# Kernel optimization log

Hardware: AMD Instinct MI355X
Metric: run time of the kernel (lower is better)

Reference implementation:

```python
import jax, jax.numpy as jnp
import numpy as np

N = 100000      # points
M = 12500       # cluster centers
E0 = 1600000    # point-level edges
E1 = 400000     # cluster-level edges
F_IN = 4        # raw point feature dim (e.g. intensity + extras)
D = 64          # hidden feature width
N_CLASSES = 8


def setup_inputs() -> dict:
    key = jax.random.key(0)
    ks = jax.random.split(key, 20)
    s = 0.05
    d = {}
    d["features"] = jax.random.normal(ks[0], (N, F_IN), jnp.float32)
    d["points"] = jax.random.normal(ks[1], (N, 3), jnp.float32)
    d["cluster_centers"] = jax.random.normal(ks[2], (M, 3), jnp.float32)
    d["l0_edges"] = jax.random.randint(ks[3], (E0, 2), 0, N)
    d["l1_edges"] = jax.random.randint(ks[4], (E1, 2), 0, M)
    d["labels"] = jax.random.randint(ks[5], (N,), 0, M)
    # Feature_extract MLP
    d["W_fe"] = s * jax.random.normal(ks[6], (F_IN + 3, D), jnp.float32)
    d["b_fe"] = jnp.zeros((D,), jnp.float32)
    # 4 Mini_GNN layers (layer2, layer2_1, layer6, layer6_1), stacked
    d["mini_We"] = s * jax.random.normal(ks[7], (4, D + 3, D), jnp.float32)
    d["mini_be"] = jnp.zeros((4, D), jnp.float32)
    d["mini_Wu"] = s * jax.random.normal(ks[8], (4, D, D), jnp.float32)
    d["mini_bu"] = jnp.zeros((4, D), jnp.float32)
    # Mini_to_Large
    d["W_m1"] = s * jax.random.normal(ks[9], (D + 3, D), jnp.float32)
    d["b_m1"] = jnp.zeros((D,), jnp.float32)
    d["W_m2"] = s * jax.random.normal(ks[10], (D, D), jnp.float32)
    d["b_m2"] = jnp.zeros((D,), jnp.float32)
    # 2 GNN layers on cluster graph (layer4, layer4_1), stacked
    d["gnn_We"] = s * jax.random.normal(ks[11], (2, D + 3, D), jnp.float32)
    d["gnn_be"] = jnp.zeros((2, D), jnp.float32)
    d["gnn_Wu"] = s * jax.random.normal(ks[12], (2, D, D), jnp.float32)
    d["gnn_bu"] = jnp.zeros((2, D), jnp.float32)
    # Large_to_Mini
    d["W_l"] = s * jax.random.normal(ks[13], (D + 3, D), jnp.float32)
    d["b_l"] = jnp.zeros((D,), jnp.float32)
    # Classifier
    d["W_c"] = s * jax.random.normal(ks[14], (D, N_CLASSES), jnp.float32)
    d["b_c"] = jnp.zeros((N_CLASSES,), jnp.float32)
    return d


def _gnn_layer(feat, pos, edges, We, be, Wu, bu, n_nodes):
    """PointGNN-style layer: gather -> edge MLP -> scatter max -> update MLP -> residual."""
    src, dst = edges[:, 0], edges[:, 1]
    e_in = jnp.concatenate([pos[src] - pos[dst], feat[src]], axis=-1)  # [E, 3+D]
    h = jax.nn.relu(e_in @ We + be)                                     # [E, D]
    agg = jax.ops.segment_max(h, dst, num_segments=n_nodes)            # [n, D]
    agg = jnp.where(jnp.isneginf(agg), 0.0, agg)  # nodes with no in-edges -> 0
    return jax.nn.relu(agg @ Wu + bu) + feat


def reference(features, points, cluster_centers, l0_edges, l1_edges, labels,
              W_fe, b_fe, mini_We, mini_be, mini_Wu, mini_bu,
              W_m1, b_m1, W_m2, b_m2, gnn_We, gnn_be, gnn_Wu, gnn_bu,
              W_l, b_l, W_c, b_c):
    rel = points - cluster_centers[labels]  # [N, 3] point pos relative to its cluster
    # layer1: Feature_extract
    f1 = jax.nn.relu(jnp.concatenate([features, rel], -1) @ W_fe + b_fe)
    # layer2 / layer2_1: Mini_GNN (scatter max) on point graph
    f2 = _gnn_layer(f1, points, l0_edges, mini_We[0], mini_be[0], mini_Wu[0], mini_bu[0], N)
    f2_1 = _gnn_layer(f2, points, l0_edges, mini_We[1], mini_be[1], mini_Wu[1], mini_bu[1], N)
    # layer3: Mini_to_Large (scatter sum by labels)
    h = jax.nn.relu(jnp.concatenate([f2_1, rel], -1) @ W_m1 + b_m1)
    c = jax.ops.segment_sum(h, labels, num_segments=M)  # [M, D]
    f3 = jax.nn.relu(c @ W_m2 + b_m2)
    # layer4 / layer4_1: GNN (scatter max) on cluster graph
    f4 = _gnn_layer(f3, cluster_centers, l1_edges, gnn_We[0], gnn_be[0], gnn_Wu[0], gnn_bu[0], M)
    f4_1 = _gnn_layer(f4, cluster_centers, l1_edges, gnn_We[1], gnn_be[1], gnn_Wu[1], gnn_bu[1], M)
    # layer5: Large_to_Mini (gather by labels)
    f5 = jax.nn.relu(jnp.concatenate([f4_1[labels], rel], -1) @ W_l + b_l)
    # layer6 / layer6_1 with residual skips per call()
    f6 = _gnn_layer(f5, points, l0_edges, mini_We[2], mini_be[2], mini_Wu[2], mini_bu[2], N)
    f6 = f6 + f2_1
    f6_1 = _gnn_layer(f6, points, l0_edges, mini_We[3], mini_be[3], mini_Wu[3], mini_bu[3], N)
    final = f6_1 + f2
    return final @ W_c + b_c  # [N, N_CLASSES] per-point logits
```

## Files before the change

kernel.cpp:

```cpp
#include <hip/hip_runtime.h>

#define N_PTS   100000
#define M_CL    12500
#define E0_N    1600000
#define E1_N    400000

#define NB      256
#define BIN_CAP 32
#define RANGE0  391
#define RANGE1  49
#define BCAP0   8192
#define BCAP1   2048

#define LSTR    72

typedef unsigned short ushortT;
typedef short  short8 __attribute__((ext_vector_type(8)));
typedef float  v4f    __attribute__((ext_vector_type(4)));
typedef _Float16 h2   __attribute__((ext_vector_type(2)));
typedef unsigned u4v  __attribute__((ext_vector_type(4)));

__device__ inline ushortT f2bf(float x){
  union{float f; unsigned u;} v; v.f = x;
  unsigned r = v.u + 0x7fffu + ((v.u >> 16) & 1u);
  return (ushortT)(r >> 16);
}
__device__ inline float bf2f(ushortT h){
  union{unsigned u; float f;} v; v.u = ((unsigned)h) << 16;
  return v.f;
}
__device__ inline ushortT f2h(float x){
  union{_Float16 h; ushortT u;} v; v.h = (_Float16)x;
  return v.u;
}
__device__ inline float h2f(ushortT u){
  union{ushortT u; _Float16 h;} v; v.u = u;
  return (float)v.h;
}
__device__ inline h2 pkmax(h2 a, h2 b){ return __builtin_elementwise_max(a, b); }
__device__ inline h2 u2h(unsigned u){ union{unsigned u; h2 h;} v{u}; return v.h; }


__global__ void k_binit(int* c0, int* c1){
  int t = threadIdx.x;
  c0[t] = t*BCAP0;
  c1[t] = t*BCAP1;
}

template<int RANGE>
__global__ __launch_bounds__(256) void k_bin(const int* __restrict__ edges, int E,
                                             int* __restrict__ bcur, unsigned* __restrict__ tmp){
  __shared__ unsigned stage[NB*BIN_CAP];
  __shared__ int scnt[NB];
  __shared__ int sbase[NB];
  int tid = threadIdx.x;
  int nchunks = (E + 2047) / 2048;
  for (int c = blockIdx.x; c < nchunks; c += gridDim.x){
    int base = c*2048;
    scnt[tid] = 0;
    __syncthreads();
    #pragma unroll
    for (int r=0;r<8;++r){
      int e = base + r*256 + tid;
      if (e < E){
        int s = edges[2*e], d = edges[2*e+1];
        int bk = d / RANGE;
        unsigned packed = ((unsigned)s << 11) | (unsigned)(d - bk*RANGE);
        int pos = atomicAdd(&scnt[bk], 1);
        if (pos < BIN_CAP) stage[bk*BIN_CAP+pos] = packed;
        else tmp[atomicAdd(&bcur[bk],1)] = packed;
      }
    }
    __syncthreads();
    {
      int nfl = scnt[tid]; if (nfl > BIN_CAP) nfl = BIN_CAP;
      sbase[tid] = atomicAdd(&bcur[tid], nfl);
    }
    __syncthreads();
    int wv = tid >> 6, ln = tid & 63;
    for (int bb=0; bb<32; ++bb){
      int bk = wv*64 + bb*2 + (ln>>5);
      int ent = ln & 31;
      int nf = scnt[bk]; if (nf > BIN_CAP) nf = BIN_CAP;
      if (ent < nf) tmp[sbase[bk]+ent] = stage[bk*BIN_CAP+ent];
    }
    __syncthreads();
  }
}

__global__ void k_scan_bases(const int* c0, int* bb0, int* off0e,
                             const int* c1, int* bb1, int* off1e){
  const int* cur = blockIdx.x ? c1 : c0;
  int* bb = blockIdx.x ? bb1 : bb0;
  int* offe = blockIdx.x ? off1e : off0e;
  int BC = blockIdx.x ? BCAP1 : BCAP0;
  int lane = threadIdx.x & 63;
  int base = lane*4;
  int v0 = cur[base+0] - (base+0)*BC;
  int v1 = cur[base+1] - (base+1)*BC;
  int v2 = cur[base+2] - (base+2)*BC;
  int v3 = cur[base+3] - (base+3)*BC;
  int psum = v0+v1+v2+v3, sc = psum;
  #pragma unroll
  for (int st=1; st<64; st<<=1){
    int x = __shfl_up(sc, st, 64);
    if (lane >= st) sc += x;
  }
  int ex = sc - psum;
  bb[base+0] = ex;
  bb[base+1] = ex + v0;
  bb[base+2] = ex + v0 + v1;
  bb[base+3] = ex + v0 + v1 + v2;
  if (lane == 63) *offe = sc;
}

template<int RANGE, int BCAP>
__global__ __launch_bounds__(256) void k_csr_build(const unsigned* __restrict__ tmp, const int* __restrict__ bcur,
                                                   const int* __restrict__ bb, int n,
                                                   int* __restrict__ offs, int* __restrict__ csr){
  constexpr int K = (RANGE + 255) / 256;
  __shared__ int hist[RANGE];
  __shared__ int part[256];
  int b = blockIdx.x, tid = threadIdx.x;
  int dlo = b*RANGE;
  int range = n - dlo; if (range > RANGE) range = RANGE; if (range < 0) range = 0;
  int cnt = bcur[b] - b*BCAP;
  for (int t=tid; t<RANGE; t+=256) hist[t] = 0;
  __syncthreads();
  const unsigned* sl = tmp + (size_t)b*BCAP;
  for (int j=tid; j<cnt; j+=256) atomicAdd(&hist[sl[j] & 2047u], 1);
  __syncthreads();
  int s = 0; int loc[K];
  #pragma unroll
  for (int kk=0; kk<K; ++kk){
    int idx = tid*K + kk;
    int v = (idx < RANGE) ? hist[idx] : 0;
    loc[kk] = s; s += v;
  }
  part[tid] = s; __syncthreads();
  int own = s;
  for (int st=1; st<256; st<<=1){
    int x = (tid >= st) ? part[tid-st] : 0;
    __syncthreads();
    part[tid] += x;
    __syncthreads();
  }
  int ebase = part[tid] - own;
  int gb = bb[b];
  __syncthreads();
  #pragma unroll
  for (int kk=0; kk<K; ++kk){
    int idx = tid*K + kk;
    if (idx < RANGE){
      int ex = ebase + loc[kk];
      if (idx < range) offs[dlo+idx] = gb + ex;
      hist[idx] = ex;
    }
  }
  __syncthreads();
  for (int j=tid; j<cnt; j+=256){
    unsigned p = sl[j];
    int pos = atomicAdd(&hist[p & 2047u], 1);
    csr[gb + pos] = (int)(p >> 11);
  }
}


__global__ __launch_bounds__(256) void k_count_lab(const int* __restrict__ labels, int n, int* __restrict__ cnt){
  int i = blockIdx.x*256 + threadIdx.x;
  if (i < n) atomicAdd(&cnt[labels[i]], 1);
}

__global__ __launch_bounds__(256) void k_chunk_sum(const int* __restrict__ cnt, int n, int* __restrict__ part){
  __shared__ int sd[256];
  int t = threadIdx.x, base = blockIdx.x*2048;
  int s = 0;
  #pragma unroll
  for (int r=0;r<8;++r){ int i = base + t*8 + r; if (i<n) s += cnt[i]; }
  sd[t]=s; __syncthreads();
  for (int st=128; st>0; st>>=1){ if (t<st) sd[t]+=sd[t+st]; __syncthreads(); }
  if (t==0) part[blockIdx.x]=sd[0];
}

__global__ void k_scan_part(int* part, int B, int* offs, int n){
  int lane = threadIdx.x & 63;
  int v = (lane < B) ? part[lane] : 0;
  int orig = v;
  #pragma unroll
  for (int st=1; st<64; st<<=1){
    int x = __shfl_up(v, st, 64);
    if (lane >= st) v += x;
  }
  if (lane < B) part[lane] = v - orig;
  if (lane == 63) offs[n] = v;
}

__global__ __launch_bounds__(256) void k_chunk_scan(const int* __restrict__ cnt, int n,
                                                    const int* __restrict__ part, int* __restrict__ offs){
  __shared__ int sd[256];
  int t=threadIdx.x, base=blockIdx.x*2048;
  int v[8]; int s=0;
  #pragma unroll
  for (int r=0;r<8;++r){ int i=base+t*8+r; v[r] = (i<n)?cnt[i]:0; s+=v[r]; }
  sd[t]=s; __syncthreads();
  for (int st=1; st<256; st<<=1){
    int x = (t>=st)? sd[t-st] : 0;
    __syncthreads();
    sd[t]+=x;
    __syncthreads();
  }
  int acc = part[blockIdx.x] + sd[t] - s;
  #pragma unroll
  for (int r=0;r<8;++r){ int i=base+t*8+r; if (i<n) offs[i]=acc; acc+=v[r]; }
}

__global__ __launch_bounds__(256) void k_fill_lab(const int* __restrict__ labels, int n,
                                                  const int* __restrict__ offs, int* __restrict__ cur,
                                                  int* __restrict__ csr){
  int i = blockIdx.x*256 + threadIdx.x;
  if (i < n){
    int d = labels[i];
    int p = atomicAdd(&cur[d], 1);
    csr[offs[d]+p] = i;
  }
}


struct WSrc { const float* p[16]; };

__global__ __launch_bounds__(256) void k_wprep(WSrc s, ushortT* __restrict__ wt, ushortT* __restrict__ wtc){
  int slot = blockIdx.x;
  if (slot < 15){
    const float* src = s.p[slot];
    ushortT* dst = wt + slot*4096;
    for (int e=threadIdx.x; e<4096; e+=256){
      int nn = e>>6, kk = e&63;
      dst[e] = f2bf(src[kk*64+nn]);
    }
  } else {
    const float* src = s.p[15];
    for (int e=threadIdx.x; e<1024; e+=256){
      int nn = e>>6, kk = e&63;
      wtc[e] = (nn<8) ? f2bf(src[kk*8+nn]) : (ushortT)0;
    }
  }
}


__global__ __launch_bounds__(256) void k_f1g(const float* __restrict__ features, const float* __restrict__ points,
                                             const float* __restrict__ centers, const int* __restrict__ labels,
                                             const float* __restrict__ W, const float* __restrict__ b,
                                             const ushortT* __restrict__ Wt2, const float* __restrict__ bias2,
                                             const float* __restrict__ Wr2,
                                             float* __restrict__ rel, ushortT* __restrict__ f1b,
                                             ushortT* __restrict__ gout, int n, int ntiles){
  __shared__ ushortT lds[4*16*LSTR];
  int tid = threadIdx.x;
  int lane = tid & 63, wslot = tid >> 6;
  int quad = lane >> 4, l15 = lane & 15;
  int gw = (blockIdx.x*256 + tid) >> 6;
  int nw = (gridDim.x*256) >> 6;
  float Wf0=W[0*64+lane], Wf1=W[1*64+lane], Wf2=W[2*64+lane], Wf3=W[3*64+lane];
  float wr0=W[4*64+lane], wr1=W[5*64+lane], wr2=W[6*64+lane];
  float bias=b[lane];
  short8 s0_0 = *(const short8*)(Wt2 + ( 0 + l15)*64 +  0 + quad*8);
  short8 s0_1 = *(const short8*)(Wt2 + ( 0 + l15)*64 + 32 + quad*8);
  short8 s1_0 = *(const short8*)(Wt2 + (16 + l15)*64 +  0 + quad*8);
  short8 s1_1 = *(const short8*)(Wt2 + (16 + l15)*64 + 32 + quad*8);
  short8 s2_0 = *(const short8*)(Wt2 + (32 + l15)*64 +  0 + quad*8);
  short8 s2_1 = *(const short8*)(Wt2 + (32 + l15)*64 + 32 + quad*8);
  short8 s3_0 = *(const short8*)(Wt2 + (48 + l15)*64 +  0 + quad*8);
  short8 s3_1 = *(const short8*)(Wt2 + (48 + l15)*64 + 32 + quad*8);
  float eb0 = bias2[l15], eb1 = bias2[16+l15], eb2 = bias2[32+l15], eb3 = bias2[48+l15];
  float e0c0=Wr2[0*64+l15], e0c1=Wr2[0*64+16+l15], e0c2=Wr2[0*64+32+l15], e0c3=Wr2[0*64+48+l15];
  float e1c0=Wr2[1*64+l15], e1c1=Wr2[1*64+16+l15], e1c2=Wr2[1*64+32+l15], e1c3=Wr2[1*64+48+l15];
  float e2c0=Wr2[2*64+l15], e2c1=Wr2[2*64+16+l15], e2c2=Wr2[2*64+32+l15], e2c3=Wr2[2*64+48+l15];

  for (int t=gw; t<ntiles; t+=nw){
    int i0 = t*16;
    for (int r=0;r<16;++r){
      int row = i0 + r;
      bool ok = row < n;
      int rr = ok ? row : n-1;
      int lb = labels[rr];
      float rx = points[rr*3+0]-centers[lb*3+0];
      float ry = points[rr*3+1]-centers[lb*3+1];
      float rz = points[rr*3+2]-centers[lb*3+2];
      float acc = bias + wr0*rx + wr1*ry + wr2*rz;
      acc += features[rr*4+0]*Wf0 + features[rr*4+1]*Wf1;
      acc += features[rr*4+2]*Wf2 + features[rr*4+3]*Wf3;
      acc = fmaxf(acc, 0.f);
      ushortT ab = f2bf(acc);
      if (ok){
        f1b[(size_t)row*64+lane] = ab;
        if (lane==0){ rel[row*3+0]=rx; rel[row*3+1]=ry; rel[row*3+2]=rz; }
      }
      lds[wslot*(16*LSTR) + r*LSTR + lane] = ab;
    }
    __builtin_amdgcn_wave_barrier();
    const ushortT* lp = lds + wslot*(16*LSTR) + l15*LSTR + quad*8;
    short8 sa0 = *(const short8*)(lp);
    short8 sa1 = *(const short8*)(lp + 32);
    __builtin_amdgcn_wave_barrier();
    v4f ec0 = {0.f,0.f,0.f,0.f}, ec1 = ec0, ec2 = ec0, ec3 = ec0;
    ec0 = __builtin_amdgcn_mfma_f32_16x16x32_bf16(sa0, s0_0, ec0, 0,0,0);
    ec1 = __builtin_amdgcn_mfma_f32_16x16x32_bf16(sa0, s1_0, ec1, 0,0,0);
    ec2 = __builtin_amdgcn_mfma_f32_16x16x32_bf16(sa0, s2_0, ec2, 0,0,0);
    ec3 = __builtin_amdgcn_mfma_f32_16x16x32_bf16(sa0, s3_0, ec3, 0,0,0);
    ec0 = __builtin_amdgcn_mfma_f32_16x16x32_bf16(sa1, s0_1, ec0, 0,0,0);
    ec1 = __builtin_amdgcn_mfma_f32_16x16x32_bf16(sa1, s1_1, ec1, 0,0,0);
    ec2 = __builtin_amdgcn_mfma_f32_16x16x32_bf16(sa1, s2_1, ec2, 0,0,0);
    ec3 = __builtin_amdgcn_mfma_f32_16x16x32_bf16(sa1, s3_1, ec3, 0,0,0);
    #pragma unroll
    for (int r=0;r<4;++r){
      int row = i0 + quad*4 + r;
      if (row < n){
        float vx=points[row*3+0], vy=points[row*3+1], vz=points[row*3+2];
        float g0 = ec0[r] + eb0 + vx*e0c0 + vy*e1c0 + vz*e2c0;
        float g1 = ec1[r] + eb1 + vx*e0c1 + vy*e1c1 + vz*e2c1;
        float g2 = ec2[r] + eb2 + vx*e0c2 + vy*e1c2 + vz*e2c2;
        float g3 = ec3[r] + eb3 + vx*e0c3 + vy*e1c3 + vz*e2c3;
        size_t base = (size_t)row*64 + l15;
        gout[base] = f2h(g0); gout[base+16] = f2h(g1); gout[base+32] = f2h(g2); gout[base+48] = f2h(g3);
      }
    }
  }
}


template<bool RELU, int NRES, bool USEREL, bool GATHER, bool OUT16, bool F16O, int EMODE, bool ERELU>
__global__ __launch_bounds__(256) void k_gemm(
    const ushortT* __restrict__ A, const ushortT* __restrict__ Wt,
    const float* __restrict__ bias, const float* __restrict__ Wr,
    const float* __restrict__ rel, const int* __restrict__ gidx,
    const ushortT* __restrict__ r1, const ushortT* __restrict__ r2,
    ushortT* __restrict__ out16,
    const ushortT* __restrict__ Wt2, const float* __restrict__ bias2,
    const float* __restrict__ Wr2, const float* __restrict__ vec2,
    void* __restrict__ eout,
    int n, int ntiles)
{
  constexpr int LDSZ = (EMODE>0) ? 4*16*LSTR : 4;
  __shared__ ushortT lds[LDSZ];
  int tid = threadIdx.x;
  int lane = tid & 63, wslot = tid >> 6;
  int quad = lane >> 4, l15 = lane & 15;
  int gw = (blockIdx.x*256 + tid) >> 6;
  int nw = (gridDim.x*256) >> 6;

  short8 bfr0_0 = *(const short8*)(Wt + ( 0 + l15)*64 +  0 + quad*8);
  short8 bfr0_1 = *(const short8*)(Wt + ( 0 + l15)*64 + 32 + quad*8);
  short8 bfr1_0 = *(const short8*)(Wt + (16 + l15)*64 +  0 + quad*8);
  short8 bfr1_1 = *(const short8*)(Wt + (16 + l15)*64 + 32 + quad*8);
  short8 bfr2_0 = *(const short8*)(Wt + (32 + l15)*64 +  0 + quad*8);
  short8 bfr2_1 = *(const short8*)(Wt + (32 + l15)*64 + 32 + quad*8);
  short8 bfr3_0 = *(const short8*)(Wt + (48 + l15)*64 +  0 + quad*8);
  short8 bfr3_1 = *(const short8*)(Wt + (48 + l15)*64 + 32 + quad*8);
  float bs0 = bias[ 0 + l15], bs1 = bias[16 + l15];
  float bs2 = bias[32 + l15], bs3 = bias[48 + l15];
  float w0c0=0,w0c1=0,w0c2=0,w0c3=0, w1c0=0,w1c1=0,w1c2=0,w1c3=0, w2c0=0,w2c1=0,w2c2=0,w2c3=0;
  if (USEREL){
    w0c0=Wr[0*64+l15]; w0c1=Wr[0*64+16+l15]; w0c2=Wr[0*64+32+l15]; w0c3=Wr[0*64+48+l15];
    w1c0=Wr[1*64+l15]; w1c1=Wr[1*64+16+l15]; w1c2=Wr[1*64+32+l15]; w1c3=Wr[1*64+48+l15];
    w2c0=Wr[2*64+l15]; w2c1=Wr[2*64+16+l15]; w2c2=Wr[2*64+32+l15]; w2c3=Wr[2*64+48+l15];
  }

  short8 s0_0{}, s0_1{}, s1_0{}, s1_1{}, s2_0{}, s2_1{}, s3_0{}, s3_1{};
  float eb0=0, eb1=0, eb2=0, eb3=0;
  float e0c0=0,e0c1=0,e0c2=0,e0c3=0, e1c0=0,e1c1=0,e1c2=0,e1c3=0, e2c0=0,e2c1=0,e2c2=0,e2c3=0;
  float ebias_c = 0.f;
  if (EMODE == 1){
    s0_0 = *(const short8*)(Wt2 + ( 0 + l15)*64 +  0 + quad*8);
    s0_1 = *(const short8*)(Wt2 + ( 0 + l15)*64 + 32 + quad*8);
    s1_0 = *(const short8*)(Wt2 + (16 + l15)*64 +  0 + quad*8);
    s1_1 = *(const short8*)(Wt2 + (16 + l15)*64 + 32 + quad*8);
    s2_0 = *(const short8*)(Wt2 + (32 + l15)*64 +  0 + quad*8);
    s2_1 = *(const short8*)(Wt2 + (32 + l15)*64 + 32 + quad*8);
    s3_0 = *(const short8*)(Wt2 + (48 + l15)*64 +  0 + quad*8);
    s3_1 = *(const short8*)(Wt2 + (48 + l15)*64 + 32 + quad*8);
    eb0 = bias2[l15]; eb1 = bias2[16+l15]; eb2 = bias2[32+l15]; eb3 = bias2[48+l15];
    e0c0=Wr2[0*64+l15]; e0c1=Wr2[0*64+16+l15]; e0c2=Wr2[0*64+32+l15]; e0c3=Wr2[0*64+48+l15];
    e1c0=Wr2[1*64+l15]; e1c1=Wr2[1*64+16+l15]; e1c2=Wr2[1*64+32+l15]; e1c3=Wr2[1*64+48+l15];
    e2c0=Wr2[2*64+l15]; e2c1=Wr2[2*64+16+l15]; e2c2=Wr2[2*64+32+l15]; e2c3=Wr2[2*64+48+l15];
  } else if (EMODE == 2){
    s0_0 = *(const short8*)(Wt2 + l15*64 +  0 + quad*8);
    s0_1 = *(const short8*)(Wt2 + l15*64 + 32 + quad*8);
    ebias_c = (l15 < 8) ? bias2[l15] : 0.f;
  }

  for (int t=gw; t<ntiles; t+=nw){
    int i0 = t*16;
    int rowA = i0 + l15; if (rowA >= n) rowA = n-1;
    if (GATHER) rowA = gidx[rowA];
    const ushortT* ap = A + (size_t)rowA*64 + quad*8;
    short8 a0 = *(const short8*)(ap);
    short8 a1 = *(const short8*)(ap + 32);
    v4f ac0 = {0.f,0.f,0.f,0.f}, ac1 = ac0, ac2 = ac0, ac3 = ac0;
    ac0 = __builtin_amdgcn_mfma_f32_16x16x32_bf16(a0, bfr0_0, ac0, 0,0,0);
    ac1 = __builtin_amdgcn_mfma_f32_16x16x32_bf16(a0, bfr1_0, ac1, 0,0,0);
    ac2 = __builtin_amdgcn_mfma_f32_16x16x32_bf16(a0, bfr2_0, ac2, 0,0,0);
    ac3 = __builtin_amdgcn_mfma_f32_16x16x32_bf16(a0, bfr3_0, ac3, 0,0,0);
    ac0 = __builtin_amdgcn_mfma_f32_16x16x32_bf16(a1, bfr0_1, ac0, 0,0,0);
    ac1 = __builtin_amdgcn_mfma_f32_16x16x32_bf16(a1, bfr1_1, ac1, 0,0,0);
    ac2 = __builtin_amdgcn_mfma_f32_16x16x32_bf16(a1, bfr2_1, ac2, 0,0,0);
    ac3 = __builtin_amdgcn_mfma_f32_16x16x32_bf16(a1, bfr3_1, ac3, 0,0,0);

    #pragma unroll
    for (int r=0;r<4;++r){
      int row = i0 + quad*4 + r;
      bool rowok = (row < n);
      float rx=0.f, ry=0.f, rz=0.f;
      if (USEREL && rowok){ rx=rel[row*3+0]; ry=rel[row*3+1]; rz=rel[row*3+2]; }
      float v0 = ac0[r] + bs0, v1 = ac1[r] + bs1, v2 = ac2[r] + bs2, v3 = ac3[r] + bs3;
      if (USEREL){
        v0 += rx*w0c0 + ry*w1c0 + rz*w2c0;
        v1 += rx*w0c1 + ry*w1c1 + rz*w2c1;
        v2 += rx*w0c2 + ry*w1c2 + rz*w2c2;
        v3 += rx*w0c3 + ry*w1c3 + rz*w2c3;
      }
      if (RELU){ v0=fmaxf(v0,0.f); v1=fmaxf(v1,0.f); v2=fmaxf(v2,0.f); v3=fmaxf(v3,0.f); }
      size_t base = (size_t)row*64 + l15;
      if (rowok){
        if (NRES>=1){
          v0 += bf2f(r1[base]); v1 += bf2f(r1[base+16]); v2 += bf2f(r1[base+32]); v3 += bf2f(r1[base+48]);
        }
        if (NRES>=2){
          v0 += bf2f(r2[base]); v1 += bf2f(r2[base+16]); v2 += bf2f(r2[base+32]); v3 += bf2f(r2[base+48]);
        }
        if (OUT16){
          if (F16O){
            out16[base] = f2h(v0); out16[base+16] = f2h(v1); out16[base+32] = f2h(v2); out16[base+48] = f2h(v3);
          } else {
            out16[base] = f2bf(v0); out16[base+16] = f2bf(v1); out16[base+32] = f2bf(v2); out16[base+48] = f2bf(v3);
          }
        }
      }
      if (EMODE > 0){
        int lb = wslot*(16*LSTR) + (quad*4+r)*LSTR + l15;
        lds[lb]      = f2bf(v0);
        lds[lb + 16] = f2bf(v1);
        lds[lb + 32] = f2bf(v2);
        lds[lb + 48] = f2bf(v3);
      }
    }

    if (EMODE > 0){
      __builtin_amdgcn_wave_barrier();
      const ushortT* lp = lds + wslot*(16*LSTR) + l15*LSTR + quad*8;
      short8 sa0 = *(const short8*)(lp);
      short8 sa1 = *(const short8*)(lp + 32);
      __builtin_amdgcn_wave_barrier();
      if (EMODE == 1){
        v4f ec0 = {0.f,0.f,0.f,0.f}, ec1 = ec0, ec2 = ec0, ec3 = ec0;
        ec0 = __builtin_amdgcn_mfma_f32_16x16x32_bf16(sa0, s0_0, ec0, 0,0,0);
        ec1 = __builtin_amdgcn_mfma_f32_16x16x32_bf16(sa0, s1_0, ec1, 0,0,0);
        ec2 = __builtin_amdgcn_mfma_f32_16x16x32_bf16(sa0, s2_0, ec2, 0,0,0);
        ec3 = __builtin_amdgcn_mfma_f32_16x16x32_bf16(sa0, s3_0, ec3, 0,0,0);
        ec0 = __builtin_amdgcn_mfma_f32_16x16x32_bf16(sa1, s0_1, ec0, 0,0,0);
        ec1 = __builtin_amdgcn_mfma_f32_16x16x32_bf16(sa1, s1_1, ec1, 0,0,0);
        ec2 = __builtin_amdgcn_mfma_f32_16x16x32_bf16(sa1, s2_1, ec2, 0,0,0);
        ec3 = __builtin_amdgcn_mfma_f32_16x16x32_bf16(sa1, s3_1, ec3, 0,0,0);
        ushortT* eo = (ushortT*)eout;
        #pragma unroll
        for (int r=0;r<4;++r){
          int row = i0 + quad*4 + r;
          if (row < n){
            float vx=vec2[row*3+0], vy=vec2[row*3+1], vz=vec2[row*3+2];
            float g0 = ec0[r] + eb0 + vx*e0c0 + vy*e1c0 + vz*e2c0;
            float g1 = ec1[r] + eb1 + vx*e0c1 + vy*e1c1 + vz*e2c1;
            float g2 = ec2[r] + eb2 + vx*e0c2 + vy*e1c2 + vz*e2c2;
            float g3 = ec3[r] + eb3 + vx*e0c3 + vy*e1c3 + vz*e2c3;
            if (ERELU){ g0=fmaxf(g0,0.f); g1=fmaxf(g1,0.f); g2=fmaxf(g2,0.f); g3=fmaxf(g3,0.f); }
            size_t base = (size_t)row*64 + l15;
            eo[base] = f2h(g0); eo[base+16] = f2h(g1); eo[base+32] = f2h(g2); eo[base+48] = f2h(g3);
          }
        }
      } else {
        v4f ec = {0.f,0.f,0.f,0.f};
        ec = __builtin_amdgcn_mfma_f32_16x16x32_bf16(sa0, s0_0, ec, 0,0,0);
        ec = __builtin_amdgcn_mfma_f32_16x16x32_bf16(sa1, s0_1, ec, 0,0,0);
        if (l15 < 8){
          float* eo = (float*)eout;
          #pragma unroll
          for (int r=0;r<4;++r){
            int row = i0 + quad*4 + r;
            if (row < n) eo[(size_t)row*8 + l15] = ec[r] + ebias_c;
          }
        }
      }
    }
  }
}


__global__ __launch_bounds__(256) void k_edge_agg(const int* __restrict__ offs, const int* __restrict__ csr,
                                                  const float* __restrict__ pos, const ushortT* __restrict__ g,
                                                  const float* __restrict__ Wp, ushortT* __restrict__ agg, int n){
  int lane = threadIdx.x & 63;
  int grp = lane >> 3, d8 = lane & 7;
  int gbase = lane & 56;
  int gw = (blockIdx.x*256 + threadIdx.x) >> 6;
  int nw = (gridDim.x*256) >> 6;
  const u4v* g4 = (const u4v*)g;
  float2 w0[4], w1[4], w2[4];
  #pragma unroll
  for (int q=0;q<4;++q){
    w0[q] = *(const float2*)(Wp + 0*64 + d8*8 + 2*q);
    w1[q] = *(const float2*)(Wp + 1*64 + 2*q + d8*8);
    w2[q] = *(const float2*)(Wp + 2*64 + d8*8 + 2*q);
  }
  const h2 NEGBIG = {(_Float16)-60000.f, (_Float16)-60000.f};
  int n8 = (n+7) >> 3;
  for (int ii=gw; ii<n8; ii+=nw){
    int i0 = ii*8;
    int ig = i0 + grp; bool ok = ig < n; if (!ok) ig = n-1;
    int b = offs[ig], e = offs[ig+1];
    int cnt = e - b, c1 = cnt - 1;
    int mx = cnt;
    mx = max(mx, __shfl_xor(mx, 8, 64));
    mx = max(mx, __shfl_xor(mx, 16, 64));
    mx = max(mx, __shfl_xor(mx, 32, 64));
    h2 m0=NEGBIG, m1=NEGBIG, m2=NEGBIG, m3=NEGBIG;
    for (int J=0; J<mx; J+=8){
      if (J < cnt){
        int sv = csr[b + min(J + d8, c1)];
        #pragma unroll
        for (int jj=0; jj<8; ++jj){
          int s = __shfl(sv, gbase + jj, 64);
          u4v u = g4[(size_t)s*8 + d8];
          m0 = pkmax(m0, u2h(u.x));
          m1 = pkmax(m1, u2h(u.y));
          m2 = pkmax(m2, u2h(u.z));
          m3 = pkmax(m3, u2h(u.w));
        }
      }
    }
    float px = pos[ig*3+0], py = pos[ig*3+1], pz = pos[ig*3+2];
    u4v outv;
    {
      float sA = w0[0].x*px + w1[0].x*py + w2[0].x*pz;
      float sB = w0[0].y*px + w1[0].y*py + w2[0].y*pz;
      outv.x = (unsigned)f2bf(fmaxf((float)m0.x - sA, 0.f)) |
               ((unsigned)f2bf(fmaxf((float)m0.y - sB, 0.f)) << 16);
    }
    {
      float sA = w0[1].x*px + w1[1].x*py + w2[1].x*pz;
      float sB = w0[1].y*px + w1[1].y*py + w2[1].y*pz;
      outv.y = (unsigned)f2bf(fmaxf((float)m1.x - sA, 0.f)) |
               ((unsigned)f2bf(fmaxf((float)m1.y - sB, 0.f)) << 16);
    }
    {
      float sA = w0[2].x*px + w1[2].x*py + w2[2].x*pz;
      float sB = w0[2].y*px + w1[2].y*py + w2[2].y*pz;
      outv.z = (unsigned)f2bf(fmaxf((float)m2.x - sA, 0.f)) |
               ((unsigned)f2bf(fmaxf((float)m2.y - sB, 0.f)) << 16);
    }
    {
      float sA = w0[3].x*px + w1[3].x*py + w2[3].x*pz;
      float sB = w0[3].y*px + w1[3].y*py + w2[3].y*pz;
      outv.w = (unsigned)f2bf(fmaxf((float)m3.x - sA, 0.f)) |
               ((unsigned)f2bf(fmaxf((float)m3.y - sB, 0.f)) << 16);
    }
    if (ok) ((u4v*)agg)[(size_t)ig*8 + d8] = outv;
  }
}


__global__ __launch_bounds__(256) void k_seg_gather(const int* __restrict__ offs, const int* __restrict__ csr,
                                                    const ushortT* __restrict__ h, ushortT* __restrict__ c, int m){
  int lane = threadIdx.x & 63;
  int wv = (blockIdx.x*256 + threadIdx.x) >> 6;
  if (wv >= m) return;
  int b = offs[wv], e = offs[wv+1];
  float acc = 0.f;
  for (int k=b; k<e; ++k){
    int i = csr[k];
    acc += h2f(h[(size_t)i*64+lane]);
  }
  c[(size_t)wv*64+lane] = f2bf(acc);
}


extern "C" void kernel_launch(void* const* d_in, const int* in_sizes, int n_in,
                              void* d_out, int out_size, void* d_ws, size_t ws_size,
                              hipStream_t stream){
  const float* features = (const float*)d_in[0];
  const float* points   = (const float*)d_in[1];
  const float* centers  = (const float*)d_in[2];
  const int*   l0e      = (const int*)d_in[3];
  const int*   l1e      = (const int*)d_in[4];
  const int*   labels   = (const int*)d_in[5];
  const float* W_fe = (const float*)d_in[6];
  const float* b_fe = (const float*)d_in[7];
  const float* mWe  = (const float*)d_in[8];
  const float* mbe  = (const float*)d_in[9];
  const float* mWu  = (const float*)d_in[10];
  const float* mbu  = (const float*)d_in[11];
  const float* W_m1 = (const float*)d_in[12];
  const float* b_m1 = (const float*)d_in[13];
  const float* W_m2 = (const float*)d_in[14];
  const float* b_m2 = (const float*)d_in[15];
  const float* gWe  = (const float*)d_in[16];
  const float* gbe  = (const float*)d_in[17];
  const float* gWu  = (const float*)d_in[18];
  const float* gbu  = (const float*)d_in[19];
  const float* W_l  = (const float*)d_in[20];
  const float* b_l  = (const float*)d_in[21];
  const float* W_c  = (const float*)d_in[22];
  const float* b_c  = (const float*)d_in[23];
  float* out = (float*)d_out;

  char* w = (char*)d_ws;
  size_t off = 0;
  auto alloc = [&](size_t bytes)->void*{
    void* p = (void*)(w + off);
    off = (off + bytes + 255) & ~(size_t)255;
    return p;
  };
  float* rel  = (float*)alloc((size_t)N_PTS*3*4);
  ushortT* UF1 = (ushortT*)alloc((size_t)N_PTS*64*2);
  ushortT* UF2 = (ushortT*)alloc((size_t)N_PTS*64*2);
  ushortT* UF21= (ushortT*)alloc((size_t)N_PTS*64*2);
  ushortT* UF5 = (ushortT*)alloc((size_t)N_PTS*64*2);
  ushortT* UF6 = (ushortT*)alloc((size_t)N_PTS*64*2);
  ushortT* gbuf= (ushortT*)alloc((size_t)N_PTS*64*2);
  ushortT* abuf= (ushortT*)alloc((size_t)N_PTS*64*2);
  ushortT* cb_b= (ushortT*)alloc((size_t)M_CL*64*2);
  ushortT* UF3 = (ushortT*)alloc((size_t)M_CL*64*2);
  ushortT* UF4 = (ushortT*)alloc((size_t)M_CL*64*2);
  ushortT* cg_b= (ushortT*)alloc((size_t)M_CL*64*2);
  ushortT* cagg_b = (ushortT*)alloc((size_t)M_CL*64*2);
  ushortT* f41_b  = (ushortT*)alloc((size_t)M_CL*64*2);
  ushortT* wt  = (ushortT*)alloc((size_t)15*4096*2);
  ushortT* wtc = (ushortT*)alloc((size_t)1024*2);
  int* offs0 = (int*)alloc((size_t)(N_PTS+1)*4);
  int* csr0  = (int*)alloc((size_t)E0_N*4);
  int* offs1 = (int*)alloc((size_t)(M_CL+1)*4);
  int* csr1  = (int*)alloc((size_t)E1_N*4);
  unsigned* tmp0 = (unsigned*)alloc((size_t)NB*BCAP0*4);
  unsigned* tmp1 = (unsigned*)alloc((size_t)NB*BCAP1*4);
  int* bcur0 = (int*)alloc(NB*4);
  int* bcur1 = (int*)alloc(NB*4);
  int* bb0   = (int*)alloc(NB*4);
  int* bb1   = (int*)alloc(NB*4);
  char* zbase = (char*)alloc(0);
  int* cntL = (int*)alloc((size_t)M_CL*4);
  int* curL = (int*)alloc((size_t)M_CL*4);
  size_t zbytes = (size_t)((char*)(w+off) - zbase);
  int* offsL = (int*)alloc((size_t)(M_CL+1)*4);
  int* csrL  = (int*)alloc((size_t)N_PTS*4);
  int* partL = (int*)alloc(64*4);
  (void)ws_size; (void)in_sizes; (void)n_in; (void)out_size;

  const int NT_N = (N_PTS+15)/16;
  const int NT_M = (M_CL +15)/16;
  const int GBG_N = 1563;
  const int GBG_M = 196;
  const int GB_N  = 3125;

  hipMemsetAsync(zbase, 0, zbytes, stream);

  k_binit<<<1, 256, 0, stream>>>(bcur0, bcur1);
  k_bin<RANGE0><<<256, 256, 0, stream>>>(l0e, E0_N, bcur0, tmp0);
  k_bin<RANGE1><<<196, 256, 0, stream>>>(l1e, E1_N, bcur1, tmp1);
  k_scan_bases<<<2, 64, 0, stream>>>(bcur0, bb0, offs0+N_PTS, bcur1, bb1, offs1+M_CL);
  k_csr_build<RANGE0,BCAP0><<<NB, 256, 0, stream>>>(tmp0, bcur0, bb0, N_PTS, offs0, csr0);
  k_csr_build<RANGE1,BCAP1><<<NB, 256, 0, stream>>>(tmp1, bcur1, bb1, M_CL, offs1, csr1);

  k_count_lab<<<(N_PTS+255)/256, 256, 0, stream>>>(labels, N_PTS, cntL);
  k_chunk_sum<<<7, 256, 0, stream>>>(cntL, M_CL, partL);
  k_scan_part<<<1, 64, 0, stream>>>(partL, 7, offsL, M_CL);
  k_chunk_scan<<<7, 256, 0, stream>>>(cntL, M_CL, partL, offsL);
  k_fill_lab<<<(N_PTS+255)/256, 256, 0, stream>>>(labels, N_PTS, offsL, curL, csrL);

  WSrc ws{};
  ws.p[0]=mWu+0*4096; ws.p[1]=mWu+1*4096; ws.p[2]=mWu+2*4096; ws.p[3]=mWu+3*4096;
  ws.p[4]=W_m2; ws.p[5]=gWu+0*4096; ws.p[6]=gWu+1*4096;
  ws.p[7]=mWe+0*4288+192; ws.p[8]=mWe+1*4288+192; ws.p[9]=mWe+2*4288+192; ws.p[10]=mWe+3*4288+192;
  ws.p[11]=W_m1; ws.p[12]=W_l; ws.p[13]=gWe+0*4288+192; ws.p[14]=gWe+1*4288+192;
  ws.p[15]=W_c;
  k_wprep<<<16, 256, 0, stream>>>(ws, wt, wtc);

  k_f1g<<<GBG_N, 256, 0, stream>>>(features, points, centers, labels, W_fe, b_fe,
      wt+7*4096, mbe+0, mWe+0*4288, rel, UF1, gbuf, N_PTS, NT_N);

  k_edge_agg<<<GB_N,256,0,stream>>>(offs0, csr0, points, gbuf, mWe+0*4288, abuf, N_PTS);
  k_gemm<true,1,false,false,true,false,1,false><<<GBG_N,256,0,stream>>>(abuf, wt+0*4096, mbu+0,
      nullptr, nullptr, nullptr, UF1, nullptr, UF2,
      wt+8*4096, mbe+64, mWe+1*4288, points, gbuf, N_PTS, NT_N);
  k_edge_agg<<<GB_N,256,0,stream>>>(offs0, csr0, points, gbuf, mWe+1*4288, abuf, N_PTS);
  k_gemm<true,1,false,false,true,false,1,true><<<GBG_N,256,0,stream>>>(abuf, wt+1*4096, mbu+64,
      nullptr, nullptr, nullptr, UF2, nullptr, UF21,
      wt+11*4096, b_m1, W_m1+4096, rel, gbuf, N_PTS, NT_N);
  k_seg_gather<<<(M_CL*64+255)/256, 256, 0, stream>>>(offsL, csrL, gbuf, cb_b, M_CL);
  k_gemm<true,0,false,false,true,false,1,false><<<GBG_M,256,0,stream>>>(cb_b, wt+4*4096, b_m2,
      nullptr, nullptr, nullptr, nullptr, nullptr, UF3,
      wt+13*4096, gbe+0, gWe+0*4288, centers, cg_b, M_CL, NT_M);
  k_edge_agg<<<GBG_M,256,0,stream>>>(offs1, csr1, centers, cg_b, gWe+0*4288, cagg_b, M_CL);
  k_gemm<true,1,false,false,true,false,1,false><<<GBG_M,256,0,stream>>>(cagg_b, wt+5*4096, gbu+0,
      nullptr, nullptr, nullptr, UF3, nullptr, UF4,
      wt+14*4096, gbe+64, gWe+1*4288, centers, cg_b, M_CL, NT_M);
  k_edge_agg<<<GBG_M,256,0,stream>>>(offs1, csr1, centers, cg_b, gWe+1*4288, cagg_b, M_CL);
  k_gemm<true,1,false,false,true,false,0,false><<<GBG_M,256,0,stream>>>(cagg_b, wt+6*4096, gbu+64,
      nullptr, nullptr, nullptr, UF4, nullptr, f41_b,
      nullptr, nullptr, nullptr, nullptr, nullptr, M_CL, NT_M);
  k_gemm<true,0,true,true,true,false,1,false><<<GBG_N,256,0,stream>>>(f41_b, wt+12*4096, b_l,
      W_l+4096, rel, labels, nullptr, nullptr, UF5,
      wt+9*4096, mbe+128, mWe+2*4288, points, gbuf, N_PTS, NT_N);
  k_edge_agg<<<GB_N,256,0,stream>>>(offs0, csr0, points, gbuf, mWe+2*4288, abuf, N_PTS);
  k_gemm<true,2,false,false,true,false,1,false><<<GBG_N,256,0,stream>>>(abuf, wt+2*4096, mbu+128,
      nullptr, nullptr, nullptr, UF5, UF21, UF6,
      wt+10*4096, mbe+192, mWe+3*4288, points, gbuf, N_PTS, NT_N);
  k_edge_agg<<<GB_N,256,0,stream>>>(offs0, csr0, points, gbuf, mWe+3*4288, abuf, N_PTS);
  k_gemm<true,2,false,false,false,false,2,false><<<GBG_N,256,0,stream>>>(abuf, wt+3*4096, mbu+192,
      nullptr, nullptr, nullptr, UF6, UF2, nullptr,
      wtc, b_c, nullptr, nullptr, out, N_PTS, NT_N);
}
```

Before: 525.4 us.

## Merge graph preprocessing kernels and build label CSR via bucketed binning

Result: faster. 485.5 us (-7.6%).

```diff
diff --git a/kernel.cpp b/kernel.cpp
--- a/kernel.cpp
+++ b/kernel.cpp
@@ -11,6 +11,7 @@
 #define RANGE1  49
 #define BCAP0   8192
 #define BCAP1   2048
+#define BCAPL   1024
 
 #define LSTR    72
 
@@ -41,21 +42,42 @@
 __device__ inline h2 u2h(unsigned u){ union{unsigned u; h2 h;} v{u}; return v.h; }
 
 
-__global__ void k_binit(int* c0, int* c1){
-  int t = threadIdx.x;
-  c0[t] = t*BCAP0;
-  c1[t] = t*BCAP1;
-}
-
-template<int RANGE>
-__global__ __launch_bounds__(256) void k_bin(const int* __restrict__ edges, int E,
-                                             int* __restrict__ bcur, unsigned* __restrict__ tmp){
-  __shared__ unsigned stage[NB*BIN_CAP];
-  __shared__ int scnt[NB];
-  __shared__ int sbase[NB];
+struct WSrc { const float* p[16]; };
+
+__global__ __launch_bounds__(256) void k_init_wprep(WSrc s, ushortT* __restrict__ wt, ushortT* __restrict__ wtc,
+                                                    int* c0, int* c1, int* cL){
+  int blk = blockIdx.x;
+  if (blk == 0){
+    int t = threadIdx.x;
+    c0[t] = t*BCAP0; c1[t] = t*BCAP1; cL[t] = t*BCAPL;
+    return;
+  }
+  int slot = blk - 1;
+  if (slot < 15){
+    const float* src = s.p[slot];
+    ushortT* dst = wt + slot*4096;
+    for (int e=threadIdx.x; e<4096; e+=256){
+      int nn = e>>6, kk = e&63;
+      dst[e] = f2bf(src[kk*64+nn]);
+    }
+  } else {
+    const float* src = s.p[15];
+    for (int e=threadIdx.x; e<1024; e+=256){
+      int nn = e>>6, kk = e&63;
+      wtc[e] = (nn<8) ? f2bf(src[kk*8+nn]) : (ushortT)0;
+    }
+  }
+}
+
+
+template<int RANGE, bool LAB>
+__device__ void bin_seg(const int* __restrict__ edges, int E,
+                        int* __restrict__ bcur, unsigned* __restrict__ tmp,
+                        int bid, int nblk,
+                        unsigned* stage, int* scnt, int* sbase){
   int tid = threadIdx.x;
   int nchunks = (E + 2047) / 2048;
-  for (int c = blockIdx.x; c < nchunks; c += gridDim.x){
+  for (int c = bid; c < nchunks; c += nblk){
     int base = c*2048;
     scnt[tid] = 0;
     __syncthreads();
@@ -63,7 +85,9 @@
     for (int r=0;r<8;++r){
       int e = base + r*256 + tid;
       if (e < E){
-        int s = edges[2*e], d = edges[2*e+1];
+        int s, d;
+        if (LAB){ s = e; d = edges[e]; }
+        else    { s = edges[2*e]; d = edges[2*e+1]; }
         int bk = d / RANGE;
         unsigned packed = ((unsigned)s << 11) | (unsigned)(d - bk*RANGE);
         int pos = atomicAdd(&scnt[bk], 1);
@@ -88,12 +112,26 @@
   }
 }
 
-__global__ void k_scan_bases(const int* c0, int* bb0, int* off0e,
-                             const int* c1, int* bb1, int* off1e){
-  const int* cur = blockIdx.x ? c1 : c0;
-  int* bb = blockIdx.x ? bb1 : bb0;
-  int* offe = blockIdx.x ? off1e : off0e;
-  int BC = blockIdx.x ? BCAP1 : BCAP0;
+__global__ __launch_bounds__(256) void k_bin_all(const int* __restrict__ l0e, const int* __restrict__ l1e,
+                                                 const int* __restrict__ labels,
+                                                 int* bc0, int* bc1, int* bcL,
+                                                 unsigned* t0, unsigned* t1, unsigned* tL){
+  __shared__ unsigned stage[NB*BIN_CAP];
+  __shared__ int scnt[NB];
+  __shared__ int sbase[NB];
+  int b = blockIdx.x;
+  if (b < 256)      bin_seg<RANGE0,false>(l0e, E0_N, bc0, t0, b, 256, stage, scnt, sbase);
+  else if (b < 452) bin_seg<RANGE1,false>(l1e, E1_N, bc1, t1, b-256, 196, stage, scnt, sbase);
+  else              bin_seg<RANGE1,true >(labels, N_PTS, bcL, tL, b-452, 49, stage, scnt, sbase);
+}
+
+__global__ void k_scan_all(const int* c0, int* bb0, int* e0,
+                           const int* c1, int* bb1, int* e1,
+                           const int* cL, int* bbL, int* eL){
+  const int* cur; int* bb; int* offe; int BC;
+  if (blockIdx.x == 0){ cur=c0; bb=bb0; offe=e0; BC=BCAP0; }
+  else if (blockIdx.x == 1){ cur=c1; bb=bb1; offe=e1; BC=BCAP1; }
+  else { cur=cL; bb=bbL; offe=eL; BC=BCAPL; }
   int lane = threadIdx.x & 63;
   int base = lane*4;
   int v0 = cur[base+0] - (base+0)*BC;
@@ -114,14 +152,12 @@
   if (lane == 63) *offe = sc;
 }
 
-template<int RANGE, int BCAP>
-__global__ __launch_bounds__(256) void k_csr_build(const unsigned* __restrict__ tmp, const int* __restrict__ bcur,
-                                                   const int* __restrict__ bb, int n,
-                                                   int* __restrict__ offs, int* __restrict__ csr){
-  constexpr int K = (RANGE + 255) / 256;
-  __shared__ int hist[RANGE];
-  __shared__ int part[256];
-  int b = blockIdx.x, tid = threadIdx.x;
+template<int RANGE, int BCAP, int K>
+__device__ void csr_build_seg(const unsigned* __restrict__ tmp, const int* __restrict__ bcur,
+                              const int* __restrict__ bb, int n,
+                              int* __restrict__ offs, int* __restrict__ csr,
+                              int b, int* hist, int* part){
+  int tid = threadIdx.x;
   int dlo = b*RANGE;
   int range = n - dlo; if (range > RANGE) range = RANGE; if (range < 0) range = 0;
   int cnt = bcur[b] - b*BCAP;
@@ -165,85 +201,16 @@
   }
 }
 
-
-__global__ __launch_bounds__(256) void k_count_lab(const int* __restrict__ labels, int n, int* __restrict__ cnt){
-  int i = blockIdx.x*256 + threadIdx.x;
-  if (i < n) atomicAdd(&cnt[labels[i]], 1);
-}
-
-__global__ __launch_bounds__(256) void k_chunk_sum(const int* __restrict__ cnt, int n, int* __restrict__ part){
-  __shared__ int sd[256];
-  int t = threadIdx.x, base = blockIdx.x*2048;
-  int s = 0;
-  #pragma unroll
-  for (int r=0;r<8;++r){ int i = base + t*8 + r; if (i<n) s += cnt[i]; }
-  sd[t]=s; __syncthreads();
-  for (int st=128; st>0; st>>=1){ if (t<st) sd[t]+=sd[t+st]; __syncthreads(); }
-  if (t==0) part[blockIdx.x]=sd[0];
-}
-
-__global__ void k_scan_part(int* part, int B, int* offs, int n){
-  int lane = threadIdx.x & 63;
-  int v = (lane < B) ? part[lane] : 0;
-  int orig = v;
-  #pragma unroll
-  for (int st=1; st<64; st<<=1){
-    int x = __shfl_up(v, st, 64);
-    if (lane >= st) v += x;
-  }
-  if (lane < B) part[lane] = v - orig;
-  if (lane == 63) offs[n] = v;
-}
-
-__global__ __launch_bounds__(256) void k_chunk_scan(const int* __restrict__ cnt, int n,
-                                                    const int* __restrict__ part, int* __restrict__ offs){
-  __shared__ int sd[256];
-  int t=threadIdx.x, base=blockIdx.x*2048;
-  int v[8]; int s=0;
-  #pragma unroll
-  for (int r=0;r<8;++r){ int i=base+t*8+r; v[r] = (i<n)?cnt[i]:0; s+=v[r]; }
-  sd[t]=s; __syncthreads();
-  for (int st=1; st<256; st<<=1){
-    int x = (t>=st)? sd[t-st] : 0;
-    __syncthreads();
-    sd[t]+=x;
-    __syncthreads();
-  }
-  int acc = part[blockIdx.x] + sd[t] - s;
-  #pragma unroll
-  for (int r=0;r<8;++r){ int i=base+t*8+r; if (i<n) offs[i]=acc; acc+=v[r]; }
-}
-
-__global__ __launch_bounds__(256) void k_fill_lab(const int* __restrict__ labels, int n,
-                                                  const int* __restrict__ offs, int* __restrict__ cur,
-                                                  int* __restrict__ csr){
-  int i = blockIdx.x*256 + threadIdx.x;
-  if (i < n){
-    int d = labels[i];
-    int p = atomicAdd(&cur[d], 1);
-    csr[offs[d]+p] = i;
-  }
-}
-
-
-struct WSrc { const float* p[16]; };
-
-__global__ __launch_bounds__(256) void k_wprep(WSrc s, ushortT* __restrict__ wt, ushortT* __restrict__ wtc){
-  int slot = blockIdx.x;
-  if (slot < 15){
-    const float* src = s.p[slot];
-    ushortT* dst = wt + slot*4096;
-    for (int e=threadIdx.x; e<4096; e+=256){
-      int nn = e>>6, kk = e&63;
-      dst[e] = f2bf(src[kk*64+nn]);
-    }
-  } else {
-    const float* src = s.p[15];
-    for (int e=threadIdx.x; e<1024; e+=256){
-      int nn = e>>6, kk = e&63;
-      wtc[e] = (nn<8) ? f2bf(src[kk*8+nn]) : (ushortT)0;
-    }
-  }
+__global__ __launch_bounds__(256) void k_build_all(
+    const unsigned* t0, const int* bc0, const int* bb0, int* offs0, int* csr0,
+    const unsigned* t1, const int* bc1, const int* bb1, int* offs1, int* csr1,
+    const unsigned* tL, const int* bcL, const int* bbL, int* offsL, int* csrL){
+  __shared__ int hist[RANGE0];
+  __shared__ int part[256];
+  int b = blockIdx.x;
+  if (b < 256)      csr_build_seg<RANGE0,BCAP0,2>(t0, bc0, bb0, N_PTS, offs0, csr0, b, hist, part);
+  else if (b < 512) csr_build_seg<RANGE1,BCAP1,1>(t1, bc1, bb1, M_CL, offs1, csr1, b-256, hist, part);
+  else              csr_build_seg<RANGE1,BCAPL,1>(tL, bcL, bbL, M_CL, offsL, csrL, b-512, hist, part);
 }
 
 
@@ -506,7 +473,7 @@
   #pragma unroll
   for (int q=0;q<4;++q){
     w0[q] = *(const float2*)(Wp + 0*64 + d8*8 + 2*q);
-    w1[q] = *(const float2*)(Wp + 1*64 + 2*q + d8*8);
+    w1[q] = *(const float2*)(Wp + 1*64 + d8*8 + 2*q);
     w2[q] = *(const float2*)(Wp + 2*64 + d8*8 + 2*q);
   }
   const h2 NEGBIG = {(_Float16)-60000.f, (_Float16)-60000.f};
@@ -637,19 +604,17 @@
   int* csr0  = (int*)alloc((size_t)E0_N*4);
   int* offs1 = (int*)alloc((size_t)(M_CL+1)*4);
   int* csr1  = (int*)alloc((size_t)E1_N*4);
+  int* offsL = (int*)alloc((size_t)(M_CL+1)*4);
+  int* csrL  = (int*)alloc((size_t)N_PTS*4);
   unsigned* tmp0 = (unsigned*)alloc((size_t)NB*BCAP0*4);
   unsigned* tmp1 = (unsigned*)alloc((size_t)NB*BCAP1*4);
+  unsigned* tmpL = (unsigned*)alloc((size_t)NB*BCAPL*4);
   int* bcur0 = (int*)alloc(NB*4);
   int* bcur1 = (int*)alloc(NB*4);
+  int* bcurL = (int*)alloc(NB*4);
   int* bb0   = (int*)alloc(NB*4);
   int* bb1   = (int*)alloc(NB*4);
-  char* zbase = (char*)alloc(0);
-  int* cntL = (int*)alloc((size_t)M_CL*4);
-  int* curL = (int*)alloc((size_t)M_CL*4);
-  size_t zbytes = (size_t)((char*)(w+off) - zbase);
-  int* offsL = (int*)alloc((size_t)(M_CL+1)*4);
-  int* csrL  = (int*)alloc((size_t)N_PTS*4);
-  int* partL = (int*)alloc(64*4);
+  int* bbL   = (int*)alloc(NB*4);
   (void)ws_size; (void)in_sizes; (void)n_in; (void)out_size;
 
   const int NT_N = (N_PTS+15)/16;
@@ -657,21 +622,6 @@
   const int GBG_N = 1563;
   const int GBG_M = 196;
   const int GB_N  = 3125;
-
-  hipMemsetAsync(zbase, 0, zbytes, stream);
-
-  k_binit<<<1, 256, 0, stream>>>(bcur0, bcur1);
-  k_bin<RANGE0><<<256, 256, 0, stream>>>(l0e, E0_N, bcur0, tmp0);
-  k_bin<RANGE1><<<196, 256, 0, stream>>>(l1e, E1_N, bcur1, tmp1);
-  k_scan_bases<<<2, 64, 0, stream>>>(bcur0, bb0, offs0+N_PTS, bcur1, bb1, offs1+M_CL);
-  k_csr_build<RANGE0,BCAP0><<<NB, 256, 0, stream>>>(tmp0, bcur0, bb0, N_PTS, offs0, csr0);
-  k_csr_build<RANGE1,BCAP1><<<NB, 256, 0, stream>>>(tmp1, bcur1, bb1, M_CL, offs1, csr1);
-
-  k_count_lab<<<(N_PTS+255)/256, 256, 0, stream>>>(labels, N_PTS, cntL);
-  k_chunk_sum<<<7, 256, 0, stream>>>(cntL, M_CL, partL);
-  k_scan_part<<<1, 64, 0, stream>>>(partL, 7, offsL, M_CL);
-  k_chunk_scan<<<7, 256, 0, stream>>>(cntL, M_CL, partL, offsL);
-  k_fill_lab<<<(N_PTS+255)/256, 256, 0, stream>>>(labels, N_PTS, offsL, curL, csrL);
 
   WSrc ws{};
   ws.p[0]=mWu+0*4096; ws.p[1]=mWu+1*4096; ws.p[2]=mWu+2*4096; ws.p[3]=mWu+3*4096;
@@ -679,7 +629,12 @@
   ws.p[7]=mWe+0*4288+192; ws.p[8]=mWe+1*4288+192; ws.p[9]=mWe+2*4288+192; ws.p[10]=mWe+3*4288+192;
   ws.p[11]=W_m1; ws.p[12]=W_l; ws.p[13]=gWe+0*4288+192; ws.p[14]=gWe+1*4288+192;
   ws.p[15]=W_c;
-  k_wprep<<<16, 256, 0, stream>>>(ws, wt, wtc);
+  k_init_wprep<<<17, 256, 0, stream>>>(ws, wt, wtc, bcur0, bcur1, bcurL);
+  k_bin_all<<<501, 256, 0, stream>>>(l0e, l1e, labels, bcur0, bcur1, bcurL, tmp0, tmp1, tmpL);
+  k_scan_all<<<3, 64, 0, stream>>>(bcur0, bb0, offs0+N_PTS, bcur1, bb1, offs1+M_CL, bcurL, bbL, offsL+M_CL);
+  k_build_all<<<768, 256, 0, stream>>>(tmp0, bcur0, bb0, offs0, csr0,
+                                       tmp1, bcur1, bb1, offs1, csr1,
+                                       tmpL, bcurL, bbL, offsL, csrL);
 
   k_f1g<<<GBG_N, 256, 0, stream>>>(features, points, centers, labels, W_fe, b_fe,
       wt+7*4096, mbe+0, mWe+0*4288, rel, UF1, gbuf, N_PTS, NT_N);
```
